# Kernel optimization log

Hardware: AMD Instinct MI355X
Metric: run time of the kernel (lower is better)

Reference implementation:

```python
import jax, jax.numpy as jnp
import numpy as np

B, S, D = 4, 2048, 1024


def setup_inputs() -> dict:
    key = jax.random.key(0)
    ks = jax.random.split(key, 9)
    scale = 1.0 / np.sqrt(D)
    x = jax.random.normal(ks[0], (B, S, D), dtype=jnp.float32)
    mask = jnp.tril(jnp.ones((S, S), dtype=jnp.int32))[None, :, :]  # causal, broadcast over batch
    Wq = jax.random.normal(ks[1], (D, D), dtype=jnp.float32) * scale
    bq = jax.random.normal(ks[2], (D,), dtype=jnp.float32) * 0.01
    Wk = jax.random.normal(ks[3], (D, D), dtype=jnp.float32) * scale
    bk = jax.random.normal(ks[4], (D,), dtype=jnp.float32) * 0.01
    Wv = jax.random.normal(ks[5], (D, D), dtype=jnp.float32) * scale
    bv = jax.random.normal(ks[6], (D,), dtype=jnp.float32) * 0.01
    Wo = jax.random.normal(ks[7], (D, D), dtype=jnp.float32) * scale
    bo = jax.random.normal(ks[8], (D,), dtype=jnp.float32) * 0.01
    return {"x": x, "mask": mask, "Wq": Wq, "bq": bq, "Wk": Wk, "bk": bk,
            "Wv": Wv, "bv": bv, "Wo": Wo, "bo": bo}


def reference(x, mask, Wq, bq, Wk, bk, Wv, bv, Wo, bo):
    # Linear projections (torch Linear: x @ W^T + b; here W stored as [in, out])
    Q = jnp.einsum('bsd,de->bse', x, Wq) + bq
    K = jnp.einsum('bsd,de->bse', x, Wk) + bk
    V = jnp.einsum('bsd,de->bse', x, Wv) + bv
    d_k = Q.shape[-1]
    scores = jnp.einsum('bqd,bkd->bqk', Q, K) / jnp.sqrt(jnp.float32(d_k))
    scores = jnp.where(mask == 0, jnp.float32(-jnp.inf), scores)
    attn_weights = jax.nn.softmax(scores, axis=-1)  # [B, S, S]
    attn_output = jnp.einsum('bqk,bkd->bqd', attn_weights, V)
    output = jnp.einsum('bsd,de->bse', attn_output, Wo) + bo
    return output, attn_weights
```

## Files before the change

### kernel.cpp

```cpp
#include <hip/hip_runtime.h>
#include <cstdint>
#include <cstddef>
#include <cmath>

typedef __bf16 bf16_t;
typedef bf16_t bf16x8 __attribute__((ext_vector_type(8)));
typedef bf16_t bf16x4 __attribute__((ext_vector_type(4)));
typedef float f32x4 __attribute__((ext_vector_type(4)));

constexpr int kB = 4;
constexpr int kS = 2048;
constexpr int kD = 1024;
constexpr int BM = 128, BN = 128, BK = 32;
constexpr int TILE_ELEMS = (BM + BN) * BK;

typedef __attribute__((address_space(1))) void as1void;
typedef __attribute__((address_space(3))) void as3void;

__device__ __forceinline__ void gload16(const void* g, void* l) {
  __builtin_amdgcn_global_load_lds((as1void*)g, (as3void*)l, 16, 0, 0);
}

__device__ __forceinline__ void gemm_mainloop(
    const bf16_t* __restrict__ A, int lda,
    const bf16_t* __restrict__ B, int ldb,
    int ksteps, bf16_t* lds, f32x4 acc[4][4]) {
  const int tid = threadIdx.x;
  const int w = tid >> 6, lane = tid & 63;
  const int srow = lane >> 2;
  const int scol = (lane & 3) << 3;
  const int wr = (w >> 1) << 6, wc = (w & 1) << 6;
  const int fr = lane & 15, kg = lane >> 4;

  const bf16_t* ga0 = A + (size_t)(w * 16 + srow) * lda + scol;
  const bf16_t* ga1 = A + (size_t)(64 + w * 16 + srow) * lda + scol;
  const bf16_t* gb0 = B + (size_t)(w * 16 + srow) * ldb + scol;
  const bf16_t* gb1 = B + (size_t)(64 + w * 16 + srow) * ldb + scol;
  const int oa0 = (w * 16) * BK;
  const int oa1 = (64 + w * 16) * BK;
  const int ob0 = BM * BK + (w * 16) * BK;
  const int ob1 = BM * BK + (64 + w * 16) * BK;

  gload16(ga0, lds + oa0);
  gload16(ga1, lds + oa1);
  gload16(gb0, lds + ob0);
  gload16(gb1, lds + ob1);
  ga0 += BK; ga1 += BK; gb0 += BK; gb1 += BK;
  __syncthreads();

  int cur = 0;
  for (int ks = 0; ks < ksteps; ++ks) {
    const int nxt = cur ^ 1;
    if (ks + 1 < ksteps) {
      bf16_t* nb = lds + nxt * TILE_ELEMS;
      gload16(ga0, nb + oa0);
      gload16(ga1, nb + oa1);
      gload16(gb0, nb + ob0);
      gload16(gb1, nb + ob1);
      ga0 += BK; ga1 += BK; gb0 += BK; gb1 += BK;
    }
    const bf16_t* cb = lds + cur * TILE_ELEMS;
    bf16x8 af[4], bfv[4];
#pragma unroll
    for (int m = 0; m < 4; ++m)
      af[m] = *(const bf16x8*)(cb + (wr + m * 16 + fr) * BK + kg * 8);
#pragma unroll
    for (int n = 0; n < 4; ++n)
      bfv[n] = *(const bf16x8*)(cb + BM * BK + (wc + n * 16 + fr) * BK + kg * 8);
#pragma unroll
    for (int m = 0; m < 4; ++m)
#pragma unroll
      for (int n = 0; n < 4; ++n)
        acc[m][n] = __builtin_amdgcn_mfma_f32_16x16x32_bf16(af[m], bfv[n],
                                                            acc[m][n], 0, 0, 0);
    __syncthreads();
    cur = nxt;
  }
}


__global__ __launch_bounds__(256)
void k_gemm_qkv(const bf16_t* __restrict__ A, const bf16_t* __restrict__ WT,
                const float* __restrict__ bq, const float* __restrict__ bk,
                const float* __restrict__ bv, bf16_t* __restrict__ Out) {
  __shared__ bf16_t lds[2 * TILE_ELEMS];
  const int which = blockIdx.x >> 3;
  const int n0 = (blockIdx.x & 7) * BN;
  const int m0 = blockIdx.y * BM;
  f32x4 acc[4][4] = {};
  gemm_mainloop(A + (size_t)m0 * kD, kD,
                WT + (size_t)which * kD * kD + (size_t)n0 * kD, kD,
                kD / BK, lds, acc);
  const float* bias = which == 0 ? bq : which == 1 ? bk : bv;
  const int tid = threadIdx.x, w = tid >> 6, lane = tid & 63;
  const int wr = (w >> 1) << 6, wc = (w & 1) << 6, fr = lane & 15, kg = lane >> 4;
  if (which < 2) {
    bf16_t* C = Out + (size_t)which * kB * kS * kD;
#pragma unroll
    for (int n = 0; n < 4; ++n) {
      const int col = n0 + wc + n * 16 + fr;
      const float bvv = bias[col];
#pragma unroll
      for (int m = 0; m < 4; ++m)
#pragma unroll
        for (int i = 0; i < 4; ++i) {
          const int row = m0 + wr + m * 16 + kg * 4 + i;
          C[(size_t)row * kD + col] = (bf16_t)(acc[m][n][i] + bvv);
        }
    }
  } else {
    bf16_t* VT = Out + (size_t)2 * kB * kS * kD;
#pragma unroll
    for (int n = 0; n < 4; ++n) {
      const int col = n0 + wc + n * 16 + fr;
      const float bvv = bias[col];
#pragma unroll
      for (int m = 0; m < 4; ++m)
#pragma unroll
        for (int i = 0; i < 4; ++i) {
          const int row = m0 + wr + m * 16 + kg * 4 + i;
          const int b = row >> 11, s = row & (kS - 1);
          VT[((size_t)b * kD + col) * kS + s] = (bf16_t)(acc[m][n][i] + bvv);
        }
    }
  }
}

__global__ __launch_bounds__(256)
void k_gemm_scores(const bf16_t* __restrict__ Q, const bf16_t* __restrict__ K,
                   float* __restrict__ Sc) {
  const int t = blockIdx.x, b = blockIdx.y;
  int by = (int)((sqrtf(8.f * t + 1.f) - 1.f) * 0.5f);
  while ((by + 1) * (by + 2) / 2 <= t) ++by;
  while (by * (by + 1) / 2 > t) --by;
  const int bx = t - by * (by + 1) / 2;
  __shared__ bf16_t lds[2 * TILE_ELEMS];
  const int m0 = by * BM, n0 = bx * BN;
  f32x4 acc[4][4] = {};
  gemm_mainloop(Q + (size_t)b * kS * kD + (size_t)m0 * kD, kD,
                K + (size_t)b * kS * kD + (size_t)n0 * kD, kD, kD / BK, lds, acc);
  float* Sb = Sc + (size_t)b * kS * kS;
  const int tid = threadIdx.x, w = tid >> 6, lane = tid & 63;
  const int wr = (w >> 1) << 6, wc = (w & 1) << 6, fr = lane & 15, kg = lane >> 4;
#pragma unroll
  for (int m = 0; m < 4; ++m)
#pragma unroll
    for (int n = 0; n < 4; ++n)
#pragma unroll
      for (int i = 0; i < 4; ++i) {
        const int row = m0 + wr + m * 16 + kg * 4 + i;
        const int col = n0 + wc + n * 16 + fr;
        Sb[(size_t)row * kS + col] = acc[m][n][i] * 0.03125f;
      }
}

__global__ __launch_bounds__(256)
void k_softmax(float* __restrict__ P, bf16_t* __restrict__ Pb) {
  const int row = blockIdx.x;
  const int q = row & (kS - 1);
  float* p = P + (size_t)row * kS;
  bf16_t* pb = Pb + (size_t)row * kS;
  const int L = q + 1;
  __shared__ float buf[kS];
  __shared__ float red[8];
  const int tid = threadIdx.x;
  float4* b4 = (float4*)buf;
  const float4* p4 = (const float4*)p;
  b4[tid] = p4[tid];
  b4[tid + 256] = p4[tid + 256];
  __syncthreads();
  float mx = -1e30f;
  for (int k = tid; k < L; k += 256) mx = fmaxf(mx, buf[k]);
#pragma unroll
  for (int s2 = 32; s2 >= 1; s2 >>= 1) mx = fmaxf(mx, __shfl_xor(mx, s2));
  if ((tid & 63) == 0) red[tid >> 6] = mx;
  __syncthreads();
  mx = fmaxf(fmaxf(red[0], red[1]), fmaxf(red[2], red[3]));
  float sm = 0.f;
  for (int k = tid; k < L; k += 256) {
    const float e = __expf(buf[k] - mx);
    buf[k] = e;
    sm += e;
  }
#pragma unroll
  for (int s2 = 32; s2 >= 1; s2 >>= 1) sm += __shfl_xor(sm, s2);
  if ((tid & 63) == 0) red[4 + (tid >> 6)] = sm;
  __syncthreads();
  const float inv = 1.f / (red[4] + red[5] + red[6] + red[7]);
  for (int k = tid; k < L; k += 256) {
    const float v = buf[k] * inv;
    p[k] = v;
    pb[k] = (bf16_t)v;
  }
  for (int k = L + tid; k < kS; k += 256) {
    p[k] = 0.f;
    pb[k] = (bf16_t)0.f;
  }
}

__global__ __launch_bounds__(256)
void k_gemm_pv(const bf16_t* __restrict__ P, const bf16_t* __restrict__ VT,
               bf16_t* __restrict__ AO) {
  const int bx = blockIdx.x, b = blockIdx.z;
  const int by = (int)gridDim.y - 1 - (int)blockIdx.y;
  __shared__ bf16_t lds[2 * TILE_ELEMS];
  const int m0 = by * BM, n0 = bx * BN;
  const int ksteps = (m0 + BM) / BK;
  f32x4 acc[4][4] = {};
  gemm_mainloop(P + (size_t)b * kS * kS + (size_t)m0 * kS, kS,
                VT + (size_t)b * kD * kS + (size_t)n0 * kS, kS, ksteps, lds, acc);
  bf16_t* AOb = AO + (size_t)b * kS * kD;
  const int tid = threadIdx.x, w = tid >> 6, lane = tid & 63;
  const int wr = (w >> 1) << 6, wc = (w & 1) << 6, fr = lane & 15, kg = lane >> 4;
#pragma unroll
  for (int m = 0; m < 4; ++m)
#pragma unroll
    for (int n = 0; n < 4; ++n)
#pragma unroll
      for (int i = 0; i < 4; ++i) {
        const int row = m0 + wr + m * 16 + kg * 4 + i;
        const int col = n0 + wc + n * 16 + fr;
        AOb[(size_t)row * kD + col] = (bf16_t)acc[m][n][i];
      }
}

__global__ __launch_bounds__(256)
void k_gemm_out(const bf16_t* __restrict__ A, const bf16_t* __restrict__ Bw,
                const float* __restrict__ bias, float* __restrict__ C) {
  __shared__ bf16_t lds[2 * TILE_ELEMS];
  const int m0 = blockIdx.y * BM, n0 = blockIdx.x * BN;
  f32x4 acc[4][4] = {};
  gemm_mainloop(A + (size_t)m0 * kD, kD, Bw + (size_t)n0 * kD, kD, kD / BK, lds, acc);
  const int tid = threadIdx.x, w = tid >> 6, lane = tid & 63;
  const int wr = (w >> 1) << 6, wc = (w & 1) << 6, fr = lane & 15, kg = lane >> 4;
#pragma unroll
  for (int n = 0; n < 4; ++n) {
    const int col = n0 + wc + n * 16 + fr;
    const float bv = bias[col];
#pragma unroll
    for (int m = 0; m < 4; ++m)
#pragma unroll
      for (int i = 0; i < 4; ++i) {
        const int row = m0 + wr + m * 16 + kg * 4 + i;
        C[(size_t)row * kD + col] = acc[m][n][i] + bv;
      }
  }
}

__global__ __launch_bounds__(256)
void k_cvt(const float* __restrict__ X, bf16_t* __restrict__ Y, size_t n4) {
  size_t i = (size_t)blockIdx.x * 256 + threadIdx.x;
  const size_t stride = (size_t)gridDim.x * 256;
  const float4* X4 = (const float4*)X;
  bf16x4* Y4 = (bf16x4*)Y;
  for (; i < n4; i += stride) {
    const float4 v = X4[i];
    bf16x4 o = {(bf16_t)v.x, (bf16_t)v.y, (bf16_t)v.z, (bf16_t)v.w};
    Y4[i] = o;
  }
}

__global__ __launch_bounds__(256)
void k_prep_w(const float* __restrict__ W0, const float* __restrict__ W1,
              const float* __restrict__ W2, const float* __restrict__ W3,
              bf16_t* __restrict__ T0, bf16_t* __restrict__ T1,
              bf16_t* __restrict__ T2, bf16_t* __restrict__ T3) {
  const float* W = blockIdx.z == 0 ? W0 : blockIdx.z == 1 ? W1 : blockIdx.z == 2 ? W2 : W3;
  bf16_t* T = blockIdx.z == 0 ? T0 : blockIdx.z == 1 ? T1 : blockIdx.z == 2 ? T2 : T3;
  __shared__ float t[32][33];
  const int tx = threadIdx.x, ty = threadIdx.y;
  const int x0 = blockIdx.x * 32, y0 = blockIdx.y * 32;
#pragma unroll
  for (int j = 0; j < 4; ++j)
    t[ty + 8 * j][tx] = W[(size_t)(y0 + ty + 8 * j) * kD + x0 + tx];
  __syncthreads();
#pragma unroll
  for (int j = 0; j < 4; ++j)
    T[(size_t)(x0 + ty + 8 * j) * kD + y0 + tx] = (bf16_t)t[tx][ty + 8 * j];
}

extern "C" void kernel_launch(void* const* d_in, const int* in_sizes, int n_in,
                              void* d_out, int out_size, void* d_ws, size_t ws_size,
                              hipStream_t stream) {
  (void)in_sizes; (void)n_in; (void)out_size; (void)ws_size;
  const float* x  = (const float*)d_in[0];
  const float* Wq = (const float*)d_in[2];
  const float* bq = (const float*)d_in[3];
  const float* Wk = (const float*)d_in[4];
  const float* bk = (const float*)d_in[5];
  const float* Wv = (const float*)d_in[6];
  const float* bv = (const float*)d_in[7];
  const float* Wo = (const float*)d_in[8];
  const float* bo = (const float*)d_in[9];

  float* out  = (float*)d_out;
  float* Pout = out + (size_t)kB * kS * kD;

  bf16_t* WqT = (bf16_t*)d_ws;
  bf16_t* WkT = WqT + (size_t)kD * kD;
  bf16_t* WvT = WkT + (size_t)kD * kD;
  bf16_t* WoT = WvT + (size_t)kD * kD;
  bf16_t* Qb  = WoT + (size_t)kD * kD;
  bf16_t* Kb  = Qb + (size_t)kB * kS * kD;
  bf16_t* VTb = Kb + (size_t)kB * kS * kD;
  bf16_t* Pb  = VTb + (size_t)kB * kS * kD;
  bf16_t* AOb = Pb + (size_t)kB * kS * kS;
  bf16_t* xb  = AOb + (size_t)kB * kS * kD;

  k_cvt<<<2048, 256, 0, stream>>>(x, xb, (size_t)kB * kS * kD / 4);
  k_prep_w<<<dim3(32, 32, 4), dim3(32, 8), 0, stream>>>(Wq, Wk, Wv, Wo, WqT, WkT, WvT, WoT);
  k_gemm_qkv<<<dim3(24, kB * kS / BM), 256, 0, stream>>>(xb, WqT, bq, bk, bv, Qb);
  k_gemm_scores<<<dim3(136, kB), 256, 0, stream>>>(Qb, Kb, Pout);
  k_softmax<<<kB * kS, 256, 0, stream>>>(Pout, Pb);
  k_gemm_pv<<<dim3(kD / BN, kS / BM, kB), 256, 0, stream>>>(Pb, VTb, AOb);
  k_gemm_out<<<dim3(kD / BN, kB * kS / BM), 256, 0, stream>>>(AOb, WoT, bo, out);
}
```

Before: 232.1 us.

## Replace 128x128 GEMMs with 256x256 8-wave pipelined GEMM mainloop and swizzle

Replaces the shared 128x128x32 double-buffered GEMM loop with a 256x256x64 tile loop run by 512 threads. The new loop stages loads up to two k-steps ahead with staggered global-to-LDS copies, explicit vmcnt waits, barriers and MFMA priority bumps. QKV and output projections get a grid swizzle for better L2 reuse, and all four GEMM kernels switch to the new tiles. Softmax now skips loading masked-out scores. Larger tiles reduce global traffic per FLOP but leave fewer blocks (e.g. 144 for scores, 128 for out) on a 256-CU device, which risks underfilling it.

Result: slower. 251.8 us (+8.5%).

```diff
diff --git a/kernel.cpp b/kernel.cpp
--- a/kernel.cpp
+++ b/kernel.cpp
@@ -11,8 +11,6 @@
 constexpr int kB = 4;
 constexpr int kS = 2048;
 constexpr int kD = 1024;
-constexpr int BM = 128, BN = 128, BK = 32;
-constexpr int TILE_ELEMS = (BM + BN) * BK;
 
 typedef __attribute__((address_space(1))) void as1void;
 typedef __attribute__((address_space(3))) void as3void;
@@ -21,90 +19,117 @@
   __builtin_amdgcn_global_load_lds((as1void*)g, (as3void*)l, 16, 0, 0);
 }
 
-__device__ __forceinline__ void gemm_mainloop(
+__device__ __forceinline__ void wgbar() {
+  asm volatile("" ::: "memory");
+  __builtin_amdgcn_s_barrier();
+  asm volatile("" ::: "memory");
+}
+
+__device__ __forceinline__ void gemm256_loop(
     const bf16_t* __restrict__ A, int lda,
     const bf16_t* __restrict__ B, int ldb,
-    int ksteps, bf16_t* lds, f32x4 acc[4][4]) {
+    int nk, bf16_t* lds, f32x4 acc[8][4]) {
   const int tid = threadIdx.x;
-  const int w = tid >> 6, lane = tid & 63;
-  const int srow = lane >> 2;
-  const int scol = (lane & 3) << 3;
-  const int wr = (w >> 1) << 6, wc = (w & 1) << 6;
-  const int fr = lane & 15, kg = lane >> 4;
-
-  const bf16_t* ga0 = A + (size_t)(w * 16 + srow) * lda + scol;
-  const bf16_t* ga1 = A + (size_t)(64 + w * 16 + srow) * lda + scol;
-  const bf16_t* gb0 = B + (size_t)(w * 16 + srow) * ldb + scol;
-  const bf16_t* gb1 = B + (size_t)(64 + w * 16 + srow) * ldb + scol;
-  const int oa0 = (w * 16) * BK;
-  const int oa1 = (64 + w * 16) * BK;
-  const int ob0 = BM * BK + (w * 16) * BK;
-  const int ob1 = BM * BK + (64 + w * 16) * BK;
-
-  gload16(ga0, lds + oa0);
-  gload16(ga1, lds + oa1);
-  gload16(gb0, lds + ob0);
-  gload16(gb1, lds + ob1);
-  ga0 += BK; ga1 += BK; gb0 += BK; gb1 += BK;
-  __syncthreads();
-
-  int cur = 0;
-  for (int ks = 0; ks < ksteps; ++ks) {
-    const int nxt = cur ^ 1;
-    if (ks + 1 < ksteps) {
-      bf16_t* nb = lds + nxt * TILE_ELEMS;
-      gload16(ga0, nb + oa0);
-      gload16(ga1, nb + oa1);
-      gload16(gb0, nb + ob0);
-      gload16(gb1, nb + ob1);
-      ga0 += BK; ga1 += BK; gb0 += BK; gb1 += BK;
+  const int wid = tid >> 6, lane = tid & 63;
+  const int wm = wid >> 2, wn = wid & 3;
+  const int fr = lane & 15, kg = (lane >> 4) & 3;
+  const int s_row = ((tid >> 7) << 4) | (tid & 15);
+  const int s_col = ((tid >> 4) & 7) << 3;
+  const bf16_t* pA = A + (size_t)s_row * lda + s_col;
+  const bf16_t* pB = B + (size_t)s_row * ldb + s_col;
+  const int ldst = wid << 9;
+
+  auto stg = [&](int tt, int op, int h, int j) {
+    const bf16_t* g = (op ? pB : pA) + (size_t)(h * 128 + j * 64) * (op ? ldb : lda)
+                      + (size_t)tt * 64;
+    bf16_t* d = lds + (((tt & 1) * 4 + op * 2 + h) * 8192) + j * 4096 + ldst;
+    gload16(g, d);
+  };
+
+#pragma unroll
+  for (int h = 0; h < 2; ++h)
+#pragma unroll
+    for (int j = 0; j < 2; ++j) { stg(0, 0, h, j); stg(0, 1, h, j); }
+  stg(1, 1, 0, 0); stg(1, 1, 0, 1); stg(1, 1, 1, 0); stg(1, 1, 1, 1);
+  stg(1, 0, 0, 0); stg(1, 0, 1, 0);
+  asm volatile("s_waitcnt vmcnt(6)" ::: "memory");
+  wgbar();
+
+  const int arow = kg * 128 + fr * 8;
+  for (int t = 0; t < nk; ++t) {
+    const bf16_t* sb = lds + (t & 1) * 32768;
+    const bf16_t* aslot = sb + wm * 8192;
+    const bf16_t* bslot = sb + (2 + (wn >> 1)) * 8192 + (wn & 1) * 4096;
+    bf16x8 bF[4][2];
+#pragma unroll
+    for (int q = 0; q < 4; ++q) {
+      bf16x8 aF[2][2];
+#pragma unroll
+      for (int mi = 0; mi < 2; ++mi)
+#pragma unroll
+        for (int ks = 0; ks < 2; ++ks)
+          aF[mi][ks] = *(const bf16x8*)(aslot + (2 * q + mi) * 1024 + ks * 512 + arow);
+      if (q == 0) {
+#pragma unroll
+        for (int n = 0; n < 4; ++n)
+#pragma unroll
+          for (int ks = 0; ks < 2; ++ks)
+            bF[n][ks] = *(const bf16x8*)(bslot + n * 1024 + ks * 512 + arow);
+      }
+      if (q == 0)      { if (t + 1 <= nk - 1) { stg(t + 1, 0, 0, 1); stg(t + 1, 0, 1, 1); } }
+      else if (q == 1) { if (t + 2 <= nk - 1) { stg(t + 2, 1, 0, 0); stg(t + 2, 1, 0, 1); } }
+      else if (q == 2) { if (t + 2 <= nk - 1) { stg(t + 2, 1, 1, 0); stg(t + 2, 1, 1, 1); } }
+      else             { if (t + 2 <= nk - 1) { stg(t + 2, 0, 0, 0); stg(t + 2, 0, 1, 0); } }
+      wgbar();
+      __builtin_amdgcn_s_setprio(1);
+#pragma unroll
+      for (int mi = 0; mi < 2; ++mi)
+#pragma unroll
+        for (int n = 0; n < 4; ++n)
+#pragma unroll
+          for (int ks = 0; ks < 2; ++ks)
+            acc[2 * q + mi][n] = __builtin_amdgcn_mfma_f32_16x16x32_bf16(
+                aF[mi][ks], bF[n][ks], acc[2 * q + mi][n], 0, 0, 0);
+      __builtin_amdgcn_s_setprio(0);
+      asm volatile("s_waitcnt lgkmcnt(0)" ::: "memory");
+      if (q == 3 && t < nk - 1) {
+        if (t + 2 <= nk - 1) asm volatile("s_waitcnt vmcnt(6)" ::: "memory");
+        else                 asm volatile("s_waitcnt vmcnt(0)" ::: "memory");
+      }
+      wgbar();
     }
-    const bf16_t* cb = lds + cur * TILE_ELEMS;
-    bf16x8 af[4], bfv[4];
-#pragma unroll
-    for (int m = 0; m < 4; ++m)
-      af[m] = *(const bf16x8*)(cb + (wr + m * 16 + fr) * BK + kg * 8);
-#pragma unroll
-    for (int n = 0; n < 4; ++n)
-      bfv[n] = *(const bf16x8*)(cb + BM * BK + (wc + n * 16 + fr) * BK + kg * 8);
-#pragma unroll
-    for (int m = 0; m < 4; ++m)
-#pragma unroll
-      for (int n = 0; n < 4; ++n)
-        acc[m][n] = __builtin_amdgcn_mfma_f32_16x16x32_bf16(af[m], bfv[n],
-                                                            acc[m][n], 0, 0, 0);
-    __syncthreads();
-    cur = nxt;
-  }
-}
-
-
-__global__ __launch_bounds__(256)
-void k_gemm_qkv(const bf16_t* __restrict__ A, const bf16_t* __restrict__ WT,
-                const float* __restrict__ bq, const float* __restrict__ bk,
-                const float* __restrict__ bv, bf16_t* __restrict__ Out) {
-  __shared__ bf16_t lds[2 * TILE_ELEMS];
-  const int which = blockIdx.x >> 3;
-  const int n0 = (blockIdx.x & 7) * BN;
-  const int m0 = blockIdx.y * BM;
-  f32x4 acc[4][4] = {};
-  gemm_mainloop(A + (size_t)m0 * kD, kD,
-                WT + (size_t)which * kD * kD + (size_t)n0 * kD, kD,
-                kD / BK, lds, acc);
+  }
+}
+
+
+__global__ __launch_bounds__(512, 2)
+void k_qkv256(const bf16_t* __restrict__ A, const bf16_t* __restrict__ WT,
+              const float* __restrict__ bq, const float* __restrict__ bk,
+              const float* __restrict__ bv, bf16_t* __restrict__ Out) {
+  __shared__ bf16_t lds[65536];
+  const int id = blockIdx.x;
+  const int swz = (id & 7) * 48 + (id >> 3);
+  const int mb = swz / 12, nb = swz % 12;
+  const int which = nb >> 2;
+  const int m0 = mb * 256, n0 = (nb & 3) * 256;
+  f32x4 acc[8][4] = {};
+  gemm256_loop(A + (size_t)m0 * kD, kD,
+               WT + (size_t)which * kD * kD + (size_t)n0 * kD, kD,
+               kD / 64, lds, acc);
   const float* bias = which == 0 ? bq : which == 1 ? bk : bv;
-  const int tid = threadIdx.x, w = tid >> 6, lane = tid & 63;
-  const int wr = (w >> 1) << 6, wc = (w & 1) << 6, fr = lane & 15, kg = lane >> 4;
+  const int lane = threadIdx.x & 63, wid = threadIdx.x >> 6;
+  const int wm = wid >> 2, wn = wid & 3, fr = lane & 15, kgr = lane >> 4;
   if (which < 2) {
     bf16_t* C = Out + (size_t)which * kB * kS * kD;
 #pragma unroll
     for (int n = 0; n < 4; ++n) {
-      const int col = n0 + wc + n * 16 + fr;
+      const int col = n0 + wn * 64 + n * 16 + fr;
       const float bvv = bias[col];
 #pragma unroll
-      for (int m = 0; m < 4; ++m)
+      for (int m = 0; m < 8; ++m)
 #pragma unroll
         for (int i = 0; i < 4; ++i) {
-          const int row = m0 + wr + m * 16 + kg * 4 + i;
+          const int row = m0 + wm * 128 + m * 16 + kgr * 4 + i;
           C[(size_t)row * kD + col] = (bf16_t)(acc[m][n][i] + bvv);
         }
     }
@@ -112,13 +137,13 @@
     bf16_t* VT = Out + (size_t)2 * kB * kS * kD;
 #pragma unroll
     for (int n = 0; n < 4; ++n) {
-      const int col = n0 + wc + n * 16 + fr;
+      const int col = n0 + wn * 64 + n * 16 + fr;
       const float bvv = bias[col];
 #pragma unroll
-      for (int m = 0; m < 4; ++m)
+      for (int m = 0; m < 8; ++m)
 #pragma unroll
         for (int i = 0; i < 4; ++i) {
-          const int row = m0 + wr + m * 16 + kg * 4 + i;
+          const int row = m0 + wm * 128 + m * 16 + kgr * 4 + i;
           const int b = row >> 11, s = row & (kS - 1);
           VT[((size_t)b * kD + col) * kS + s] = (bf16_t)(acc[m][n][i] + bvv);
         }
@@ -126,32 +151,85 @@
   }
 }
 
-__global__ __launch_bounds__(256)
-void k_gemm_scores(const bf16_t* __restrict__ Q, const bf16_t* __restrict__ K,
-                   float* __restrict__ Sc) {
+__global__ __launch_bounds__(512, 2)
+void k_scores256(const bf16_t* __restrict__ Q, const bf16_t* __restrict__ K,
+                 float* __restrict__ Sc) {
   const int t = blockIdx.x, b = blockIdx.y;
   int by = (int)((sqrtf(8.f * t + 1.f) - 1.f) * 0.5f);
   while ((by + 1) * (by + 2) / 2 <= t) ++by;
   while (by * (by + 1) / 2 > t) --by;
   const int bx = t - by * (by + 1) / 2;
-  __shared__ bf16_t lds[2 * TILE_ELEMS];
-  const int m0 = by * BM, n0 = bx * BN;
-  f32x4 acc[4][4] = {};
-  gemm_mainloop(Q + (size_t)b * kS * kD + (size_t)m0 * kD, kD,
-                K + (size_t)b * kS * kD + (size_t)n0 * kD, kD, kD / BK, lds, acc);
+  __shared__ bf16_t lds[65536];
+  const int m0 = by * 256, n0 = bx * 256;
+  f32x4 acc[8][4] = {};
+  gemm256_loop(Q + (size_t)b * kS * kD + (size_t)m0 * kD, kD,
+               K + (size_t)b * kS * kD + (size_t)n0 * kD, kD, kD / 64, lds, acc);
   float* Sb = Sc + (size_t)b * kS * kS;
-  const int tid = threadIdx.x, w = tid >> 6, lane = tid & 63;
-  const int wr = (w >> 1) << 6, wc = (w & 1) << 6, fr = lane & 15, kg = lane >> 4;
-#pragma unroll
-  for (int m = 0; m < 4; ++m)
-#pragma unroll
-    for (int n = 0; n < 4; ++n)
+  const int lane = threadIdx.x & 63, wid = threadIdx.x >> 6;
+  const int wm = wid >> 2, wn = wid & 3, fr = lane & 15, kgr = lane >> 4;
+#pragma unroll
+  for (int n = 0; n < 4; ++n) {
+    const int col = n0 + wn * 64 + n * 16 + fr;
+#pragma unroll
+    for (int m = 0; m < 8; ++m)
 #pragma unroll
       for (int i = 0; i < 4; ++i) {
-        const int row = m0 + wr + m * 16 + kg * 4 + i;
-        const int col = n0 + wc + n * 16 + fr;
+        const int row = m0 + wm * 128 + m * 16 + kgr * 4 + i;
         Sb[(size_t)row * kS + col] = acc[m][n][i] * 0.03125f;
       }
+  }
+}
+
+__global__ __launch_bounds__(512, 2)
+void k_pv256(const bf16_t* __restrict__ P, const bf16_t* __restrict__ VT,
+             bf16_t* __restrict__ AO) {
+  const int bx = blockIdx.x, b = blockIdx.z;
+  const int by = (int)gridDim.y - 1 - (int)blockIdx.y;
+  __shared__ bf16_t lds[65536];
+  const int m0 = by * 256, n0 = bx * 256;
+  const int nk = (m0 + 256) / 64;
+  f32x4 acc[8][4] = {};
+  gemm256_loop(P + (size_t)b * kS * kS + (size_t)m0 * kS, kS,
+               VT + (size_t)b * kD * kS + (size_t)n0 * kS, kS, nk, lds, acc);
+  bf16_t* AOb = AO + (size_t)b * kS * kD;
+  const int lane = threadIdx.x & 63, wid = threadIdx.x >> 6;
+  const int wm = wid >> 2, wn = wid & 3, fr = lane & 15, kgr = lane >> 4;
+#pragma unroll
+  for (int n = 0; n < 4; ++n) {
+    const int col = n0 + wn * 64 + n * 16 + fr;
+#pragma unroll
+    for (int m = 0; m < 8; ++m)
+#pragma unroll
+      for (int i = 0; i < 4; ++i) {
+        const int row = m0 + wm * 128 + m * 16 + kgr * 4 + i;
+        AOb[(size_t)row * kD + col] = (bf16_t)acc[m][n][i];
+      }
+  }
+}
+
+__global__ __launch_bounds__(512, 2)
+void k_out256(const bf16_t* __restrict__ A, const bf16_t* __restrict__ Bw,
+              const float* __restrict__ bias, float* __restrict__ C) {
+  __shared__ bf16_t lds[65536];
+  const int id = blockIdx.x;
+  const int swz = (id & 7) * 16 + (id >> 3);
+  const int m0 = (swz >> 2) * 256, n0 = (swz & 3) * 256;
+  f32x4 acc[8][4] = {};
+  gemm256_loop(A + (size_t)m0 * kD, kD, Bw + (size_t)n0 * kD, kD, kD / 64, lds, acc);
+  const int lane = threadIdx.x & 63, wid = threadIdx.x >> 6;
+  const int wm = wid >> 2, wn = wid & 3, fr = lane & 15, kgr = lane >> 4;
+#pragma unroll
+  for (int n = 0; n < 4; ++n) {
+    const int col = n0 + wn * 64 + n * 16 + fr;
+    const float bvv = bias[col];
+#pragma unroll
+    for (int m = 0; m < 8; ++m)
+#pragma unroll
+      for (int i = 0; i < 4; ++i) {
+        const int row = m0 + wm * 128 + m * 16 + kgr * 4 + i;
+        C[(size_t)row * kD + col] = acc[m][n][i] + bvv;
+      }
+  }
 }
 
 __global__ __launch_bounds__(256)
@@ -166,8 +244,8 @@
   const int tid = threadIdx.x;
   float4* b4 = (float4*)buf;
   const float4* p4 = (const float4*)p;
-  b4[tid] = p4[tid];
-  b4[tid + 256] = p4[tid + 256];
+  if (tid * 4 < L) b4[tid] = p4[tid];
+  if (1024 + tid * 4 < L) b4[tid + 256] = p4[tid + 256];
   __syncthreads();
   float mx = -1e30f;
   for (int k = tid; k < L; k += 256) mx = fmaxf(mx, buf[k]);
@@ -195,55 +273,6 @@
   for (int k = L + tid; k < kS; k += 256) {
     p[k] = 0.f;
     pb[k] = (bf16_t)0.f;
-  }
-}
-
-__global__ __launch_bounds__(256)
-void k_gemm_pv(const bf16_t* __restrict__ P, const bf16_t* __restrict__ VT,
-               bf16_t* __restrict__ AO) {
-  const int bx = blockIdx.x, b = blockIdx.z;
-  const int by = (int)gridDim.y - 1 - (int)blockIdx.y;
-  __shared__ bf16_t lds[2 * TILE_ELEMS];
-  const int m0 = by * BM, n0 = bx * BN;
-  const int ksteps = (m0 + BM) / BK;
-  f32x4 acc[4][4] = {};
-  gemm_mainloop(P + (size_t)b * kS * kS + (size_t)m0 * kS, kS,
-                VT + (size_t)b * kD * kS + (size_t)n0 * kS, kS, ksteps, lds, acc);
-  bf16_t* AOb = AO + (size_t)b * kS * kD;
-  const int tid = threadIdx.x, w = tid >> 6, lane = tid & 63;
-  const int wr = (w >> 1) << 6, wc = (w & 1) << 6, fr = lane & 15, kg = lane >> 4;
-#pragma unroll
-  for (int m = 0; m < 4; ++m)
-#pragma unroll
-    for (int n = 0; n < 4; ++n)
-#pragma unroll
-      for (int i = 0; i < 4; ++i) {
-        const int row = m0 + wr + m * 16 + kg * 4 + i;
-        const int col = n0 + wc + n * 16 + fr;
-        AOb[(size_t)row * kD + col] = (bf16_t)acc[m][n][i];
-      }
-}
-
-__global__ __launch_bounds__(256)
-void k_gemm_out(const bf16_t* __restrict__ A, const bf16_t* __restrict__ Bw,
-                const float* __restrict__ bias, float* __restrict__ C) {
-  __shared__ bf16_t lds[2 * TILE_ELEMS];
-  const int m0 = blockIdx.y * BM, n0 = blockIdx.x * BN;
-  f32x4 acc[4][4] = {};
-  gemm_mainloop(A + (size_t)m0 * kD, kD, Bw + (size_t)n0 * kD, kD, kD / BK, lds, acc);
-  const int tid = threadIdx.x, w = tid >> 6, lane = tid & 63;
-  const int wr = (w >> 1) << 6, wc = (w & 1) << 6, fr = lane & 15, kg = lane >> 4;
-#pragma unroll
-  for (int n = 0; n < 4; ++n) {
-    const int col = n0 + wc + n * 16 + fr;
-    const float bv = bias[col];
-#pragma unroll
-    for (int m = 0; m < 4; ++m)
-#pragma unroll
-      for (int i = 0; i < 4; ++i) {
-        const int row = m0 + wr + m * 16 + kg * 4 + i;
-        C[(size_t)row * kD + col] = acc[m][n][i] + bv;
-      }
   }
 }
 
@@ -309,9 +338,9 @@
 
   k_cvt<<<2048, 256, 0, stream>>>(x, xb, (size_t)kB * kS * kD / 4);
   k_prep_w<<<dim3(32, 32, 4), dim3(32, 8), 0, stream>>>(Wq, Wk, Wv, Wo, WqT, WkT, WvT, WoT);
-  k_gemm_qkv<<<dim3(24, kB * kS / BM), 256, 0, stream>>>(xb, WqT, bq, bk, bv, Qb);
-  k_gemm_scores<<<dim3(136, kB), 256, 0, stream>>>(Qb, Kb, Pout);
+  k_qkv256<<<384, 512, 0, stream>>>(xb, WqT, bq, bk, bv, Qb);
+  k_scores256<<<dim3(36, kB), 512, 0, stream>>>(Qb, Kb, Pout);
   k_softmax<<<kB * kS, 256, 0, stream>>>(Pout, Pb);
-  k_gemm_pv<<<dim3(kD / BN, kS / BM, kB), 256, 0, stream>>>(Pb, VTb, AOb);
-  k_gemm_out<<<dim3(kD / BN, kB * kS / BM), 256, 0, stream>>>(AOb, WoT, bo, out);
-}
+  k_pv256<<<dim3(4, 8, kB), 512, 0, stream>>>(Pb, VTb, AOb);
+  k_out256<<<128, 512, 0, stream>>>(AOb, WoT, bo, out);
+}
```
